# Kernel optimization log

Measured on AMD Instinct MI355X. Metric: run time of the kernel, lower is better.

The kernel has to match this reference:

```python
import jax, jax.numpy as jnp
import numpy as np

N_NODES = 100000
N_EDGES = 1600000
IN_C, HID_C, OUT_C = 128, 64, 40


def setup_inputs() -> dict:
    key = jax.random.key(0)
    ks = jax.random.split(key, 8)
    x = jax.random.normal(ks[0], (N_NODES, IN_C), dtype=jnp.float32)
    edge_index = jax.random.randint(ks[1], (2, N_EDGES), 0, N_NODES, dtype=jnp.int64)
    # Glorot-ish init for weights
    W1 = jax.random.normal(ks[2], (IN_C, HID_C), dtype=jnp.float32) / np.sqrt(IN_C)
    W2 = jax.random.normal(ks[3], (HID_C, HID_C), dtype=jnp.float32) / np.sqrt(HID_C)
    W3 = jax.random.normal(ks[4], (HID_C, OUT_C), dtype=jnp.float32) / np.sqrt(HID_C)
    b1 = jnp.zeros((HID_C,), jnp.float32)
    b2 = jnp.zeros((HID_C,), jnp.float32)
    b3 = jnp.zeros((OUT_C,), jnp.float32)
    return {"x": x, "edge_index": edge_index, "W1": W1, "b1": b1,
            "W2": W2, "b2": b2, "W3": W3, "b3": b3}


def _gcn_prep(edge_index, num_nodes):
    # PyG GCNConv: add self-loops, symmetric normalization with edge_weight=1.
    src = jnp.concatenate([edge_index[0], jnp.arange(num_nodes, dtype=edge_index.dtype)])
    dst = jnp.concatenate([edge_index[1], jnp.arange(num_nodes, dtype=edge_index.dtype)])
    deg = jax.ops.segment_sum(jnp.ones_like(dst, dtype=jnp.float32), dst,
                              num_segments=num_nodes)
    dis = jnp.where(deg > 0, jax.lax.rsqrt(deg), 0.0)  # deg^-1/2, inf->0
    norm = dis[src] * dis[dst]  # per-edge symmetric norm
    return src, dst, norm


def _gcn_conv(x, W, b, src, dst, norm, num_nodes):
    h = x @ W                                # [N, F_out], linear (no bias)
    msg = h[src] * norm[:, None]             # gather + scale, [E_total, F_out]
    out = jax.ops.segment_sum(msg, dst, num_segments=num_nodes)
    return out + b                           # conv bias after aggregation


def reference(x, edge_index, W1, b1, W2, b2, W3, b3):
    n = x.shape[0]
    src, dst, norm = _gcn_prep(edge_index, n)
    h = jax.nn.relu(_gcn_conv(x, W1, b1, src, dst, norm, n))
    h = jax.nn.relu(_gcn_conv(h, W2, b2, src, dst, norm, n))
    h = _gcn_conv(h, W3, b3, src, dst, norm, n)
    return jax.nn.log_softmax(h, axis=1)
```

## Files before the change

kernel.cpp:

```cpp
#include <hip/hip_runtime.h>
#include <cstdint>
#include <cstddef>
#include <math.h>

#define NN 100000
#define NE 1600000
#define NB ((NN + 255) / 256)
#define EB 400
#define EPB (NE / EB)
#define CAP 5120

#define GT_NODES 128
#define GT_KC 32
#define GT_STRIDE 132

typedef unsigned short u16;

__device__ __forceinline__ float bf2f(u16 u) {
    union { unsigned i; float f; } c; c.i = ((unsigned)u) << 16; return c.f;
}
__device__ __forceinline__ u16 f2bf(float f) {
    union { float f; unsigned int i; } c; c.f = f;
    unsigned int lsb = (c.i >> 16) & 1u;
    return (u16)((c.i + 0x7fffu + lsb) >> 16);
}
__device__ __forceinline__ unsigned int pack2(float a, float b) {
    return (unsigned int)f2bf(a) | ((unsigned int)f2bf(b) << 16);
}

__device__ __forceinline__ int load_idx(const void* ei, int isI64, int pos) {
    if (isI64) return (int)((const long long*)ei)[pos];
    return ((const int*)ei)[pos];
}

__global__ __launch_bounds__(256) void k_build(const void* __restrict__ ei,
                                               int* __restrict__ cursor,
                                               int* __restrict__ csr_tmp) {
    __shared__ int sbuf[EPB];
    __shared__ int dbuf[EPB];
    __shared__ int cnt[NB];
    __shared__ int basel[NB];
    __shared__ int anynz;

    const int* p = (const int*)ei;
    if (threadIdx.x == 0) anynz = 0;
    for (int i = threadIdx.x; i < NB; i += 256) cnt[i] = 0;
    __syncthreads();
    int nz = 0;
    for (int i = threadIdx.x; i < 1024; i += 256) nz |= (p[2 * i + 1] != 0);
    if (nz) anynz = 1;
    __syncthreads();
    int isI64 = (anynz == 0);

    int base = blockIdx.x * EPB;
    for (int i = threadIdx.x; i < EPB; i += 256) {
        int s = load_idx(ei, isI64, base + i);
        int d = load_idx(ei, isI64, NE + base + i);
        sbuf[i] = s;
        dbuf[i] = d;
        atomicAdd(&cnt[d >> 8], 1);
    }
    __syncthreads();
    for (int j = threadIdx.x; j < NB; j += 256) {
        int c = cnt[j];
        int g = c ? atomicAdd(&cursor[j], c) : 0;
        basel[j] = j * CAP + g;
        cnt[j] = 0;
    }
    __syncthreads();
    for (int i = threadIdx.x; i < EPB; i += 256) {
        int s = sbuf[i];
        int d = dbuf[i];
        int bkt = d >> 8;
        int slot = basel[bkt] + atomicAdd(&cnt[bkt], 1);
        csr_tmp[slot] = ((d & 255) << 17) | s;
    }
}

__global__ __launch_bounds__(256) void k_sort(const int* __restrict__ cursor,
                                              const int* __restrict__ csr_tmp,
                                              int* __restrict__ csr,
                                              int* __restrict__ deg,
                                              int* __restrict__ offs,
                                              float* __restrict__ dis) {
    __shared__ int h[256];
    __shared__ int sc[256];
    __shared__ int cur[256];
    int j = blockIdx.x;
    int s0 = j * CAP, s1 = s0 + cursor[j];
    h[threadIdx.x] = 0;
    __syncthreads();
    for (int p = s0 + threadIdx.x; p < s1; p += 256)
        atomicAdd(&h[csr_tmp[p] >> 17], 1);
    __syncthreads();
    int v = h[threadIdx.x];
    sc[threadIdx.x] = v;
    __syncthreads();
#pragma unroll
    for (int off = 1; off < 256; off <<= 1) {
        int u = (threadIdx.x >= off) ? sc[threadIdx.x - off] : 0;
        __syncthreads();
        sc[threadIdx.x] += u;
        __syncthreads();
    }
    int excl = sc[threadIdx.x] - v;
    int node = j * 256 + threadIdx.x;
    if (node < NN) {
        deg[node] = v;
        offs[node] = s0 + excl;
        dis[node] = rsqrtf((float)(v + 1));
    }
    cur[threadIdx.x] = excl;
    __syncthreads();
    for (int p = s0 + threadIdx.x; p < s1; p += 256) {
        int pk = csr_tmp[p];
        int dl = pk >> 17;
        int pos = s0 + atomicAdd(&cur[dl], 1);
        csr[pos] = pk & 0x1FFFF;
    }
}

template <int K, int FR, bool RELU>
__global__ __launch_bounds__(512) void k_gemm(const float* __restrict__ x,
                                              const float* __restrict__ W,
                                              const float* __restrict__ dis,
                                              u16* __restrict__ out) {
    __shared__ float xT[GT_KC * GT_STRIDE];
    __shared__ float Wc[GT_KC * 64];
    const int tid = threadIdx.x;
    const int r = tid >> 4;
    const int c = tid & 15;
    const int f4 = tid & 7;
    const int nrow = tid >> 3;
    const int nbase = blockIdx.x * GT_NODES;

    float acc[4][4];
#pragma unroll
    for (int i = 0; i < 4; ++i)
#pragma unroll
        for (int j = 0; j < 4; ++j) acc[i][j] = 0.f;

    for (int kc = 0; kc < K; kc += GT_KC) {
#pragma unroll
        for (int q = 0; q < 4; ++q) {
            int e = q * 512 + tid;
            int kk = e >> 6, j = e & 63;
            Wc[kk * 64 + j] = (j < FR) ? W[(size_t)(kc + kk) * FR + j] : 0.f;
        }
#pragma unroll
        for (int q = 0; q < 2; ++q) {
            int nl = q * 64 + nrow;
            int n = nbase + nl;
            float4 v = make_float4(0.f, 0.f, 0.f, 0.f);
            if (n < NN) v = *(const float4*)(x + (size_t)n * K + kc + f4 * 4);
            if (RELU) {
                v.x = fmaxf(v.x, 0.f); v.y = fmaxf(v.y, 0.f);
                v.z = fmaxf(v.z, 0.f); v.w = fmaxf(v.w, 0.f);
            }
            xT[(f4 * 4 + 0) * GT_STRIDE + nl] = v.x;
            xT[(f4 * 4 + 1) * GT_STRIDE + nl] = v.y;
            xT[(f4 * 4 + 2) * GT_STRIDE + nl] = v.z;
            xT[(f4 * 4 + 3) * GT_STRIDE + nl] = v.w;
        }
        __syncthreads();
#pragma unroll 8
        for (int kk = 0; kk < GT_KC; ++kk) {
            float4 a = *(const float4*)&xT[kk * GT_STRIDE + r * 4];
            float4 w = *(const float4*)&Wc[kk * 64 + c * 4];
            float xa[4] = {a.x, a.y, a.z, a.w};
            float wb[4] = {w.x, w.y, w.z, w.w};
#pragma unroll
            for (int i = 0; i < 4; ++i)
#pragma unroll
                for (int j = 0; j < 4; ++j)
                    acc[i][j] = fmaf(xa[i], wb[j], acc[i][j]);
        }
        __syncthreads();
    }
    if (c * 4 < FR) {
#pragma unroll
        for (int i = 0; i < 4; ++i) {
            int n = nbase + r * 4 + i;
            if (n < NN) {
                float dv = dis[n];
                uint2 o;
                o.x = pack2(dv * acc[i][0], dv * acc[i][1]);
                o.y = pack2(dv * acc[i][2], dv * acc[i][3]);
                *(uint2*)(out + (size_t)n * FR + c * 4) = o;
            }
        }
    }
}

template <int F, int B, bool MASK>
__device__ __forceinline__ float2 gb2(int myidx, int i, int lim, int eh,
                                      const u16* __restrict__ g, unsigned fp) {
    unsigned off[B / 2];
#pragma unroll
    for (int k = 0; k < B / 2; ++k) {
        int s = __shfl(myidx, i + 2 * k + eh);
        off[k] = (unsigned)s * (unsigned)(F * 2) + fp * 4u;
    }
    unsigned hv[B / 2];
#pragma unroll
    for (int k = 0; k < B / 2; ++k)
        hv[k] = *(const unsigned*)((const char*)g + off[k]);
    float x0 = 0.f, x1 = 0.f, y0 = 0.f, y1 = 0.f;
#pragma unroll
    for (int k = 0; k < B / 2; ++k) {
        float vx = bf2f((u16)(hv[k] & 0xffffu));
        float vy = bf2f((u16)(hv[k] >> 16));
        if (MASK) {
            bool ok = (i + 2 * k + eh) < lim;
            vx = ok ? vx : 0.f;
            vy = ok ? vy : 0.f;
        }
        if (k & 1) { x1 += vx; y1 += vy; }
        else       { x0 += vx; y0 += vy; }
    }
    float2 r; r.x = x0 + x1; r.y = y0 + y1; return r;
}

template <int F, bool SOFTMAX>
__global__ __launch_bounds__(256) void k_gather2(const int* __restrict__ offs,
                                                 const int* __restrict__ deg,
                                                 const int* __restrict__ csr,
                                                 const float* __restrict__ dis,
                                                 const u16* __restrict__ g,
                                                 const float* __restrict__ b,
                                                 float* __restrict__ out) {
    int n = blockIdx.x * 4 + (threadIdx.x >> 6);
    unsigned lane = threadIdx.x & 63;
    unsigned fc2 = lane & 31;
    int eh = (int)(lane >> 5);
    bool valid = (2u * fc2 < (unsigned)F);
    unsigned fp = valid ? fc2 : (unsigned)(F / 2 - 1);

    int start = __builtin_amdgcn_readfirstlane(offs[n]);
    int len   = __builtin_amdgcn_readfirstlane(deg[n]);
    float dvn = dis[n];

    unsigned sv = *(const unsigned*)((const char*)g
                      + (size_t)(unsigned)n * (unsigned)(F * 2) + fp * 4u);
    float2 acc;
    acc.x = eh ? 0.f : bf2f((u16)(sv & 0xffffu));
    acc.y = eh ? 0.f : bf2f((u16)(sv >> 16));

    int myidx = 0;
    if ((int)lane < len) myidx = csr[start + (int)lane];
    int lim = (len < 64) ? len : 64;

    if (lim > 0) {
        float2 t;
        if (lim >= 33) {
            int i = 0;
            for (; i + 16 <= lim; i += 16) {
                t = gb2<F, 16, false>(myidx, i, lim, eh, g, fp);
                acc.x += t.x; acc.y += t.y;
            }
            if (i < lim) {
                t = gb2<F, 16, true>(myidx, i, lim, eh, g, fp);
                acc.x += t.x; acc.y += t.y;
            }
        } else if (lim >= 17) {
            t = gb2<F, 32, true>(myidx, 0, lim, eh, g, fp);
            acc.x += t.x; acc.y += t.y;
        } else if (lim == 16) {
            t = gb2<F, 16, false>(myidx, 0, lim, eh, g, fp);
            acc.x += t.x; acc.y += t.y;
        } else {
            t = gb2<F, 16, true>(myidx, 0, lim, eh, g, fp);
            acc.x += t.x; acc.y += t.y;
        }
    }
    if (len > 64) {
        for (int i = 64 + eh; i < len; i += 2) {
            int s = csr[start + i];
            unsigned hv = *(const unsigned*)((const char*)g
                              + (unsigned)s * (unsigned)(F * 2) + fp * 4u);
            acc.x += bf2f((u16)(hv & 0xffffu));
            acc.y += bf2f((u16)(hv >> 16));
        }
    }
    acc.x += __shfl_xor(acc.x, 32);
    acc.y += __shfl_xor(acc.y, 32);

    float vx = dvn * acc.x + b[2 * fp + 0];
    float vy = dvn * acc.y + b[2 * fp + 1];

    if (!SOFTMAX) {
        if (eh == 0 && valid) {
            float2 o; o.x = vx; o.y = vy;
            *(float2*)(out + (size_t)n * F + 2 * fp) = o;
        }
    } else {
        float m = valid ? fmaxf(vx, vy) : -INFINITY;
#pragma unroll
        for (int off = 16; off; off >>= 1) m = fmaxf(m, __shfl_xor(m, off));
        float ex = valid ? (__expf(vx - m) + __expf(vy - m)) : 0.f;
        float sum = ex;
#pragma unroll
        for (int off = 16; off; off >>= 1) sum += __shfl_xor(sum, off);
        if (eh == 0 && valid) {
            float ls = logf(sum);
            float2 o; o.x = vx - m - ls; o.y = vy - m - ls;
            *(float2*)(out + (size_t)n * F + 2 * fp) = o;
        }
    }
}

extern "C" void kernel_launch(void* const* d_in, const int* in_sizes, int n_in,
                              void* d_out, int out_size, void* d_ws, size_t ws_size,
                              hipStream_t stream) {
    const float* x  = (const float*)d_in[0];
    const void*  ei = d_in[1];
    const float* W1 = (const float*)d_in[2];
    const float* b1 = (const float*)d_in[3];
    const float* W2 = (const float*)d_in[4];
    const float* b2 = (const float*)d_in[5];
    const float* W3 = (const float*)d_in[6];
    const float* b3 = (const float*)d_in[7];
    float* out = (float*)d_out;

    char* ws = (char*)d_ws;
    size_t off = 0;
    auto alloc = [&](size_t bytes) { void* p = ws + off; off += (bytes + 255) & ~255ULL; return p; };
    int*   cursor  = (int*)alloc(NB * 4);
    int*   deg     = (int*)alloc(NN * 4);
    float* dis     = (float*)alloc(NN * 4);
    int*   offs    = (int*)alloc(NN * 4);
    int*   csr_tmp = (int*)alloc((size_t)NB * CAP * 4);
    int*   csr     = (int*)alloc((size_t)NB * CAP * 4);
    u16*   gbuf    = (u16*)alloc((size_t)NN * 64 * 2);
    float* act     = (float*)alloc((size_t)NN * 64 * 4);

    hipMemsetAsync(cursor, 0, NB * 4, stream);
    k_build<<<EB, 256, 0, stream>>>(ei, cursor, csr_tmp);
    k_sort<<<NB, 256, 0, stream>>>(cursor, csr_tmp, csr, deg, offs, dis);

    const int gemm_grid = (NN + GT_NODES - 1) / GT_NODES;
    const int gather_grid = NN / 4;

    k_gemm<128, 64, false><<<gemm_grid, 512, 0, stream>>>(x, W1, dis, gbuf);
    k_gather2<64, false><<<gather_grid, 256, 0, stream>>>(offs, deg, csr, dis, gbuf, b1, act);

    k_gemm<64, 64, true><<<gemm_grid, 512, 0, stream>>>(act, W2, dis, gbuf);
    k_gather2<64, false><<<gather_grid, 256, 0, stream>>>(offs, deg, csr, dis, gbuf, b2, act);

    k_gemm<64, 40, true><<<gemm_grid, 512, 0, stream>>>(act, W3, dis, gbuf);
    k_gather2<40, true><<<gather_grid, 256, 0, stream>>>(offs, deg, csr, dis, gbuf, b3, out);
}
```

Baseline: 328.3 us.

## Replace FP32 FMA GEMM with split-bf16 MFMA matrix-core GEMM

```diff
diff --git a/kernel.cpp b/kernel.cpp
--- a/kernel.cpp
+++ b/kernel.cpp
@@ -10,11 +10,11 @@
 #define EPB (NE / EB)
 #define CAP 5120
 
-#define GT_NODES 128
-#define GT_KC 32
-#define GT_STRIDE 132
+#define MS 40
 
 typedef unsigned short u16;
+typedef __attribute__((ext_vector_type(8))) short bf16x8;
+typedef __attribute__((ext_vector_type(4))) float f32x4;
 
 __device__ __forceinline__ float bf2f(u16 u) {
     union { unsigned i; float f; } c; c.i = ((unsigned)u) << 16; return c.f;
@@ -23,9 +23,6 @@
     union { float f; unsigned int i; } c; c.f = f;
     unsigned int lsb = (c.i >> 16) & 1u;
     return (u16)((c.i + 0x7fffu + lsb) >> 16);
-}
-__device__ __forceinline__ unsigned int pack2(float a, float b) {
-    return (unsigned int)f2bf(a) | ((unsigned int)f2bf(b) << 16);
 }
 
 __device__ __forceinline__ int load_idx(const void* ei, int isI64, int pos) {
@@ -121,72 +118,86 @@
 }
 
 template <int K, int FR, bool RELU>
-__global__ __launch_bounds__(512) void k_gemm(const float* __restrict__ x,
-                                              const float* __restrict__ W,
-                                              const float* __restrict__ dis,
-                                              u16* __restrict__ out) {
-    __shared__ float xT[GT_KC * GT_STRIDE];
-    __shared__ float Wc[GT_KC * 64];
+__global__ __launch_bounds__(512) void k_gemm_m(const float* __restrict__ x,
+                                                const float* __restrict__ W,
+                                                const float* __restrict__ dis,
+                                                u16* __restrict__ out) {
+    __shared__ u16 Ah[128 * MS];
+    __shared__ u16 Al[128 * MS];
+    __shared__ u16 Bw[64 * MS];
     const int tid = threadIdx.x;
-    const int r = tid >> 4;
-    const int c = tid & 15;
-    const int f4 = tid & 7;
-    const int nrow = tid >> 3;
-    const int nbase = blockIdx.x * GT_NODES;
-
-    float acc[4][4];
-#pragma unroll
-    for (int i = 0; i < 4; ++i)
-#pragma unroll
-        for (int j = 0; j < 4; ++j) acc[i][j] = 0.f;
-
-    for (int kc = 0; kc < K; kc += GT_KC) {
-#pragma unroll
-        for (int q = 0; q < 4; ++q) {
-            int e = q * 512 + tid;
-            int kk = e >> 6, j = e & 63;
-            Wc[kk * 64 + j] = (j < FR) ? W[(size_t)(kc + kk) * FR + j] : 0.f;
-        }
-#pragma unroll
-        for (int q = 0; q < 2; ++q) {
-            int nl = q * 64 + nrow;
-            int n = nbase + nl;
-            float4 v = make_float4(0.f, 0.f, 0.f, 0.f);
-            if (n < NN) v = *(const float4*)(x + (size_t)n * K + kc + f4 * 4);
+    const int w = tid >> 6;
+    const int l = tid & 63;
+    const int row16 = l & 15;
+    const int kg = l >> 4;
+    const int nbase = blockIdx.x * 128;
+
+    f32x4 acc[4];
+#pragma unroll
+    for (int t = 0; t < 4; ++t) acc[t] = (f32x4){0.f, 0.f, 0.f, 0.f};
+
+    for (int kc = 0; kc < K; kc += 32) {
+        {
+            int r = tid >> 2;
+            int cg = tid & 3;
+            int n = nbase + r;
+            float vs[8];
+#pragma unroll
+            for (int j = 0; j < 8; ++j) vs[j] = 0.f;
+            if (n < NN) {
+                const float* xp = x + (size_t)n * K + kc + cg * 8;
+                float4 v0 = *(const float4*)xp;
+                float4 v1 = *(const float4*)(xp + 4);
+                vs[0] = v0.x; vs[1] = v0.y; vs[2] = v0.z; vs[3] = v0.w;
+                vs[4] = v1.x; vs[5] = v1.y; vs[6] = v1.z; vs[7] = v1.w;
+            }
             if (RELU) {
-                v.x = fmaxf(v.x, 0.f); v.y = fmaxf(v.y, 0.f);
-                v.z = fmaxf(v.z, 0.f); v.w = fmaxf(v.w, 0.f);
-            }
-            xT[(f4 * 4 + 0) * GT_STRIDE + nl] = v.x;
-            xT[(f4 * 4 + 1) * GT_STRIDE + nl] = v.y;
-            xT[(f4 * 4 + 2) * GT_STRIDE + nl] = v.z;
-            xT[(f4 * 4 + 3) * GT_STRIDE + nl] = v.w;
+#pragma unroll
+                for (int j = 0; j < 8; ++j) vs[j] = fmaxf(vs[j], 0.f);
+            }
+            u16* ah = &Ah[r * MS + cg * 8];
+            u16* al = &Al[r * MS + cg * 8];
+#pragma unroll
+            for (int j = 0; j < 8; j += 2) {
+                u16 h0 = f2bf(vs[j]);
+                u16 h1 = f2bf(vs[j + 1]);
+                float r0 = vs[j] - bf2f(h0);
+                float r1 = vs[j + 1] - bf2f(h1);
+                *(unsigned*)&ah[j] = (unsigned)h0 | ((unsigned)h1 << 16);
+                *(unsigned*)&al[j] = (unsigned)f2bf(r0) | ((unsigned)f2bf(r1) << 16);
+            }
+        }
+        {
+            int k = tid >> 4;
+            int c0 = (tid & 15) * 4;
+#pragma unroll
+            for (int j = 0; j < 4; ++j) {
+                int c = c0 + j;
+                float wv = (c < FR) ? W[(size_t)(kc + k) * FR + c] : 0.f;
+                Bw[c * MS + k] = f2bf(wv);
+            }
         }
         __syncthreads();
-#pragma unroll 8
-        for (int kk = 0; kk < GT_KC; ++kk) {
-            float4 a = *(const float4*)&xT[kk * GT_STRIDE + r * 4];
-            float4 w = *(const float4*)&Wc[kk * 64 + c * 4];
-            float xa[4] = {a.x, a.y, a.z, a.w};
-            float wb[4] = {w.x, w.y, w.z, w.w};
-#pragma unroll
-            for (int i = 0; i < 4; ++i)
-#pragma unroll
-                for (int j = 0; j < 4; ++j)
-                    acc[i][j] = fmaf(xa[i], wb[j], acc[i][j]);
+        bf16x8 ah = *(const bf16x8*)&Ah[(w * 16 + row16) * MS + kg * 8];
+        bf16x8 al = *(const bf16x8*)&Al[(w * 16 + row16) * MS + kg * 8];
+#pragma unroll
+        for (int t = 0; t < 4; ++t) {
+            bf16x8 b = *(const bf16x8*)&Bw[(t * 16 + row16) * MS + kg * 8];
+            acc[t] = __builtin_amdgcn_mfma_f32_16x16x32_bf16(ah, b, acc[t], 0, 0, 0);
+            acc[t] = __builtin_amdgcn_mfma_f32_16x16x32_bf16(al, b, acc[t], 0, 0, 0);
         }
         __syncthreads();
     }
-    if (c * 4 < FR) {
-#pragma unroll
-        for (int i = 0; i < 4; ++i) {
-            int n = nbase + r * 4 + i;
-            if (n < NN) {
-                float dv = dis[n];
-                uint2 o;
-                o.x = pack2(dv * acc[i][0], dv * acc[i][1]);
-                o.y = pack2(dv * acc[i][2], dv * acc[i][3]);
-                *(uint2*)(out + (size_t)n * FR + c * 4) = o;
+#pragma unroll
+    for (int r = 0; r < 4; ++r) {
+        int n = nbase + w * 16 + kg * 4 + r;
+        if (n < NN) {
+            float dv = dis[n];
+#pragma unroll
+            for (int t = 0; t < 4; ++t) {
+                int feat = t * 16 + row16;
+                if (feat < FR)
+                    out[(size_t)n * FR + feat] = f2bf(dv * acc[t][r]);
             }
         }
     }
@@ -338,15 +349,15 @@
     k_build<<<EB, 256, 0, stream>>>(ei, cursor, csr_tmp);
     k_sort<<<NB, 256, 0, stream>>>(cursor, csr_tmp, csr, deg, offs, dis);
 
-    const int gemm_grid = (NN + GT_NODES - 1) / GT_NODES;
+    const int gemm_grid = (NN + 127) / 128;
     const int gather_grid = NN / 4;
 
-    k_gemm<128, 64, false><<<gemm_grid, 512, 0, stream>>>(x, W1, dis, gbuf);
+    k_gemm_m<128, 64, false><<<gemm_grid, 512, 0, stream>>>(x, W1, dis, gbuf);
     k_gather2<64, false><<<gather_grid, 256, 0, stream>>>(offs, deg, csr, dis, gbuf, b1, act);
 
-    k_gemm<64, 64, true><<<gemm_grid, 512, 0, stream>>>(act, W2, dis, gbuf);
+    k_gemm_m<64, 64, true><<<gemm_grid, 512, 0, stream>>>(act, W2, dis, gbuf);
     k_gather2<64, false><<<gather_grid, 256, 0, stream>>>(offs, deg, csr, dis, gbuf, b2, act);
 
-    k_gemm<64, 40, true><<<gemm_grid, 512, 0, stream>>>(act, W3, dis, gbuf);
+    k_gemm_m<64, 40, true><<<gemm_grid, 512, 0, stream>>>(act, W3, dis, gbuf);
     k_gather2<40, true><<<gather_grid, 256, 0, stream>>>(offs, deg, csr, dis, gbuf, b3, out);
 }
```

New measurement: 287.6 us. 12.4% less time.
